# Kernel optimization log

Hardware: AMD Instinct MI355X
Metric: run time of the kernel (lower is better)

Reference implementation:

```python
import jax, jax.numpy as jnp
import numpy as np

N_RES = 768
C = 128  # act_dim == num_intermediate_channel
EPS = 1e-5


def _layer_norm(x, w, b):
    mu = jnp.mean(x, axis=-1, keepdims=True)
    var = jnp.mean(jnp.square(x - mu), axis=-1, keepdims=True)
    return (x - mu) * jax.lax.rsqrt(var + EPS) * w + b


def _linear(x, w, b):
    # torch Linear: w is [out, in]
    return jnp.einsum('ijc,dc->ijd', x, w) + b


def setup_inputs() -> dict:
    key = jax.random.key(0)
    ks = jax.random.split(key, 16)
    s = 1.0 / np.sqrt(C)
    d = {
        'act': jax.random.normal(ks[0], (N_RES, N_RES, C), jnp.float32),
        'mask': jnp.ones((N_RES, N_RES), jnp.float32),
        'ln_in_w': jnp.ones((C,), jnp.float32),
        'ln_in_b': jnp.zeros((C,), jnp.float32),
        'lp_w': jax.random.normal(ks[1], (C, C), jnp.float32) * s,
        'lp_b': jnp.zeros((C,), jnp.float32),
        'rp_w': jax.random.normal(ks[2], (C, C), jnp.float32) * s,
        'rp_b': jnp.zeros((C,), jnp.float32),
        'lg_w': jax.random.normal(ks[3], (C, C), jnp.float32) * s,
        'lg_b': jnp.ones((C,), jnp.float32),
        'rg_w': jax.random.normal(ks[4], (C, C), jnp.float32) * s,
        'rg_b': jnp.ones((C,), jnp.float32),
        'cln_w': jnp.ones((C,), jnp.float32),
        'cln_b': jnp.zeros((C,), jnp.float32),
        'op_w': jax.random.normal(ks[5], (C, C), jnp.float32) * s,
        'op_b': jnp.zeros((C,), jnp.float32),
        'gl_w': jax.random.normal(ks[6], (C, C), jnp.float32) * s,
        'gl_b': jnp.ones((C,), jnp.float32),
    }
    return d


def reference(act, mask, ln_in_w, ln_in_b, lp_w, lp_b, rp_w, rp_b,
              lg_w, lg_b, rg_w, rg_b, cln_w, cln_b, op_w, op_b, gl_w, gl_b):
    m = mask[..., None]                                   # [N, N, 1]
    act_ln = _layer_norm(act, ln_in_w, ln_in_b)           # [N, N, C]
    left = m * _linear(act_ln, lp_w, lp_b) * jax.nn.sigmoid(_linear(act_ln, lg_w, lg_b))
    right = m * _linear(act_ln, rp_w, rp_b) * jax.nn.sigmoid(_linear(act_ln, rg_w, rg_b))
    # outgoing-edges triangle multiplication
    out = jnp.einsum('ikc,jkc->ijc', left, right)          # [N, N, C]
    out = _layer_norm(out, cln_w, cln_b)
    out = _linear(out, op_w, op_b)
    gate = jax.nn.sigmoid(_linear(act_ln, gl_w, gl_b))
    return out * gate
```

## Files before the change

kernel.cpp:

```cpp
#include <hip/hip_runtime.h>
#include <hip/hip_bf16.h>
#include <math.h>


#define NRES 768
#define CD 128
#define NN (768 * 768)
#define PS2 (NN + 128)
#define PS4 (NN + 64)

typedef unsigned short u16;
typedef unsigned int u32;
typedef __attribute__((ext_vector_type(8))) short bf16x8;
typedef __attribute__((ext_vector_type(4))) float f32x4;

__device__ __forceinline__ float b2f(u16 u) {
  union { u32 i; float f; } v; v.i = ((u32)u) << 16; return v.f;
}
__device__ __forceinline__ u16 f2bf(float f) {
  __hip_bfloat16 h = __float2bfloat16(f);
  return *reinterpret_cast<u16*>(&h);
}
__device__ __forceinline__ float sigm(float x) {
  return __builtin_amdgcn_rcpf(1.0f + __builtin_amdgcn_exp2f(x * -1.44269504f));
}

__device__ __forceinline__ void async16(u16* lds, const u16* g) {
  __builtin_amdgcn_global_load_lds((const __attribute__((address_space(1))) void*)g,
                                   (__attribute__((address_space(3))) void*)lds, 16, 0, 0);
}

__device__ __forceinline__ void lds_fence() {
  asm volatile("s_waitcnt lgkmcnt(0)" ::: "memory");
  __builtin_amdgcn_sched_barrier(0);
}

__global__ void k_convw(const float* __restrict__ a, const float* __restrict__ b,
                        const float* __restrict__ c, const float* __restrict__ d,
                        const float* __restrict__ e, const float* __restrict__ f,
                        u16* __restrict__ wb) {
  int i = blockIdx.x * 256 + threadIdx.x;
  int m = i >> 14, r = i & 16383;
  const float* s = (m == 0) ? a : (m == 1) ? b : (m == 2) ? c : (m == 3) ? d : (m == 4) ? e : f;
  wb[i] = f2bf(s[r]);
}

__global__ __launch_bounds__(256, 3) void k_proj(
    const float* __restrict__ act, const float* __restrict__ mask,
    const float* __restrict__ lnw, const float* __restrict__ lnb,
    const u16* __restrict__ wb,
    const float* __restrict__ lpb, const float* __restrict__ lgb,
    const float* __restrict__ rpb, const float* __restrict__ rgb,
    const float* __restrict__ glb,
    u16* __restrict__ left_t, u16* __restrict__ right_t, u16* __restrict__ gate) {
  __shared__ u16 sx[128][128];
  __shared__ u16 stb[128 * 74];
  __shared__ float fmask[128];
  const int t = threadIdx.x;
  const int pos0 = blockIdx.x * 128;
  const int l = t & 63, w = t >> 6;
  const int lr = l & 15, g4 = l >> 4;

  {
    const int r = t >> 1, q = t & 1;
    const float* arow = act + (size_t)(pos0 + r) * CD + q * 64;
    float4 xv[16];
    float s = 0.f, ss = 0.f;
#pragma unroll
    for (int j = 0; j < 16; ++j) {
      xv[j] = *(const float4*)(arow + j * 4);
      s += xv[j].x + xv[j].y + xv[j].z + xv[j].w;
      ss += xv[j].x * xv[j].x + xv[j].y * xv[j].y + xv[j].z * xv[j].z + xv[j].w * xv[j].w;
    }
    s += __shfl_xor(s, 1); ss += __shfl_xor(ss, 1);
    float mu = s * (1.0f / CD);
    float rs = rsqrtf(ss * (1.0f / CD) - mu * mu + 1e-5f);
    const int key = (r & 7) << 3;
#pragma unroll
    for (int j = 0; j < 16; j += 2) {
      u16 o[8] __attribute__((aligned(16)));
      const float* xx = (const float*)&xv[j];
      int c0 = q * 64 + j * 4;
#pragma unroll
      for (int e2 = 0; e2 < 8; ++e2)
        o[e2] = f2bf((xx[e2] - mu) * rs * lnw[c0 + e2] + lnb[c0 + e2]);
      *(bf16x8*)&sx[r][c0 ^ key] = *(const bf16x8*)o;
    }
    if (t < 128) fmask[t] = mask[pos0 + t];
  }
  __syncthreads();

  auto pair_pass = [&](const u16* __restrict__ WP, const u16* __restrict__ WG,
                       const float* __restrict__ bP, const float* __restrict__ bG,
                       u16* __restrict__ dst) {
    bf16x8 bp[2][4], bg[2][4];
    float biasP[2], biasG[2];
    int dd[2];
#pragma unroll
    for (int c2 = 0; c2 < 2; ++c2) {
      dd[c2] = w * 32 + c2 * 16 + lr;
#pragma unroll
      for (int kk = 0; kk < 4; ++kk) {
        bp[c2][kk] = *(const bf16x8*)&WP[dd[c2] * CD + kk * 32 + g4 * 8];
        bg[c2][kk] = *(const bf16x8*)&WG[dd[c2] * CD + kk * 32 + g4 * 8];
      }
      biasP[c2] = bP[dd[c2]];
      biasG[c2] = bG[dd[c2]];
    }
#pragma unroll
    for (int mc = 0; mc < 2; ++mc) {
      lds_fence();
#pragma unroll
      for (int m = 0; m < 4; ++m) {
        const int row = mc * 64 + m * 16 + lr;
        const int key = (row & 7) << 3;
        bf16x8 af[4];
#pragma unroll
        for (int kk = 0; kk < 4; ++kk)
          af[kk] = *(const bf16x8*)&sx[row][(kk * 32 + g4 * 8) ^ key];
        const int rowc = m * 16 + g4 * 4;
        float fm[4];
#pragma unroll
        for (int r = 0; r < 4; ++r) fm[r] = fmask[mc * 64 + rowc + r];
#pragma unroll
        for (int c2 = 0; c2 < 2; ++c2) {
          f32x4 aP = {0.f, 0.f, 0.f, 0.f}, aG = {0.f, 0.f, 0.f, 0.f};
#pragma unroll
          for (int kk = 0; kk < 4; ++kk) {
            aP = __builtin_amdgcn_mfma_f32_16x16x32_bf16(af[kk], bp[c2][kk], aP, 0, 0, 0);
            aG = __builtin_amdgcn_mfma_f32_16x16x32_bf16(af[kk], bg[c2][kk], aG, 0, 0, 0);
          }
          u16 o[4] __attribute__((aligned(8)));
#pragma unroll
          for (int r = 0; r < 4; ++r)
            o[r] = f2bf((aP[r] + biasP[c2]) * sigm(aG[r] + biasG[c2]) * fm[r]);
          *(uint2*)&stb[dd[c2] * 74 + rowc] = *(const uint2*)o;
        }
      }
      lds_fence();
#pragma unroll
      for (int it = 0; it < 4; ++it) {
        const int d = w * 32 + it * 8 + (l >> 3), off = (l & 7) * 8;
        *(bf16x8*)&dst[(size_t)d * PS2 + pos0 + mc * 64 + off] = *(const bf16x8*)&stb[d * 74 + off];
      }
    }
  };

  pair_pass(wb, wb + 16384, lpb, lgb, left_t);
  pair_pass(wb + 2 * 16384, wb + 3 * 16384, rpb, rgb, right_t);

  __syncthreads();

  {
    const u16* WG = wb + 4 * 16384;
    bf16x8 bg[2][4];
    float biasG[2];
    int dd[2];
#pragma unroll
    for (int c2 = 0; c2 < 2; ++c2) {
      dd[c2] = w * 32 + c2 * 16 + lr;
#pragma unroll
      for (int kk = 0; kk < 4; ++kk)
        bg[c2][kk] = *(const bf16x8*)&WG[dd[c2] * CD + kk * 32 + g4 * 8];
      biasG[c2] = glb[dd[c2]];
    }
#pragma unroll
    for (int mc = 0; mc < 2; ++mc) {
#pragma unroll
      for (int m = 0; m < 4; ++m) {
        const int row = mc * 64 + m * 16 + lr;
        const int key = (row & 7) << 3;
        bf16x8 af[4];
#pragma unroll
        for (int kk = 0; kk < 4; ++kk)
          af[kk] = *(const bf16x8*)&sx[row][(kk * 32 + g4 * 8) ^ key];
        const int rowc = m * 16 + g4 * 4;
#pragma unroll
        for (int c2 = 0; c2 < 2; ++c2) {
          f32x4 aG = {0.f, 0.f, 0.f, 0.f};
#pragma unroll
          for (int kk = 0; kk < 4; ++kk)
            aG = __builtin_amdgcn_mfma_f32_16x16x32_bf16(af[kk], bg[c2][kk], aG, 0, 0, 0);
#pragma unroll
          for (int r = 0; r < 4; ++r)
            stb[(rowc + r) * 136 + dd[c2]] = f2bf(sigm(aG[r] + biasG[c2]));
        }
      }
      __syncthreads();
      {
        const int row = t >> 2, dc = (t & 3) * 32;
#pragma unroll
        for (int jj = 0; jj < 4; ++jj)
          *(bf16x8*)&gate[(size_t)(pos0 + mc * 64 + row) * CD + dc + jj * 8] =
              *(const bf16x8*)&stb[row * 136 + dc + jj * 8];
      }
      __syncthreads();
    }
  }
}

__global__ __launch_bounds__(256, 4) void k_tri(
    const u16* __restrict__ left_t, const u16* __restrict__ right_t,
    float* __restrict__ o1, float* __restrict__ o2, float* __restrict__ o3,
    int cbase) {
  __shared__ u16 sA[2][128 * 32];
  __shared__ u16 sB[2][128 * 32];
  const int t = threadIdx.x, l = t & 63, w = t >> 6;
  const int bid = blockIdx.x;
  const int xcd = bid & 7, idx = bid >> 3;
  const int c = cbase + xcd * 8 + idx / 36;
  const int tile = idx - (idx / 36) * 36;
  const int ti = tile / 6, tj = tile - (tile / 6) * 6;
  const u16* A = left_t + (size_t)c * PS2 + (size_t)ti * 128 * NRES;
  const u16* B = right_t + (size_t)c * PS2 + (size_t)tj * 128 * NRES;
  const int lr = l & 15, cj = l >> 4;
  const int wr = (w >> 1) * 64, wc = (w & 1) * 64;
  const int wbase = t & ~63;
  f32x4 acc[4][4];
#pragma unroll
  for (int m = 0; m < 4; ++m)
#pragma unroll
    for (int n = 0; n < 4; ++n) acc[m][n] = (f32x4){0.f, 0.f, 0.f, 0.f};

  auto stage = [&](int p, int k0) {
#pragma unroll
    for (int it = 0; it < 2; ++it) {
      int li = it * 256 + t;
      int row = li >> 2, ch = li & 3;
      int cs = ch ^ ((row >> 1) & 3);
      async16(&sA[p][(it * 256 + wbase) * 8], A + (size_t)row * NRES + k0 + cs * 8);
      async16(&sB[p][(it * 256 + wbase) * 8], B + (size_t)row * NRES + k0 + cs * 8);
    }
  };

  stage(0, 0);
  __syncthreads();
  for (int ks = 0; ks < 24; ++ks) {
    const int p = ks & 1;
    if (ks < 23) stage(p ^ 1, (ks + 1) * 32);
    bf16x8 av[4], bv[4];
#pragma unroll
    for (int m = 0; m < 4; ++m) {
      const int row = wr + m * 16 + lr;
      av[m] = *(const bf16x8*)&sA[p][row * 32 + ((cj ^ ((row >> 1) & 3)) * 8)];
    }
#pragma unroll
    for (int n = 0; n < 4; ++n) {
      const int row = wc + n * 16 + lr;
      bv[n] = *(const bf16x8*)&sB[p][row * 32 + ((cj ^ ((row >> 1) & 3)) * 8)];
    }
#pragma unroll
    for (int m = 0; m < 4; ++m)
#pragma unroll
      for (int n = 0; n < 4; ++n)
        acc[m][n] = __builtin_amdgcn_mfma_f32_16x16x32_bf16(av[m], bv[n], acc[m][n], 0, 0, 0);
    __syncthreads();
  }

  float* O = (c < 64) ? (o1 + (size_t)c * PS4)
           : (c < 96) ? (o2 + (size_t)(c - 64) * PS4)
                      : (o3 + (size_t)(c - 96) * PS4);
  const int r0l = (l >> 4) << 2;
#pragma unroll
  for (int m = 0; m < 4; ++m) {
#pragma unroll
    for (int n = 0; n < 4; ++n) {
      int row = ti * 128 + wr + m * 16 + r0l;
      int col = tj * 128 + wc + n * 16 + lr;
#pragma unroll
      for (int r = 0; r < 4; ++r)
        O[(size_t)(row + r) * NRES + col] = acc[m][n][r];
    }
  }
}

__global__ __launch_bounds__(256, 2) void k_post(
    const float* __restrict__ o1, const float* __restrict__ o2, const float* __restrict__ o3,
    const u16* __restrict__ gate,
    const float* __restrict__ clnw, const float* __restrict__ clnb,
    const u16* __restrict__ wop, const float* __restrict__ opb,
    float* __restrict__ out) {
  __shared__ u16 sx[256][128];
  __shared__ float ps[4][256];
  __shared__ float pss[4][256];
  __shared__ float mu_s[256], rs_s[256];
  const int t = threadIdx.x;
  const int pos0 = blockIdx.x * 256;
  const int l = t & 63, w = t >> 6;

  {
    const float* wbase = (w < 2) ? (o1 + (size_t)(w * 32) * PS4)
                       : (w == 2) ? o2 : o3;
    float s[4] = {0.f, 0.f, 0.f, 0.f}, ss[4] = {0.f, 0.f, 0.f, 0.f};
#pragma unroll
    for (int pp = 0; pp < 32; ++pp) {
      const float4 v = *(const float4*)&wbase[(size_t)pp * PS4 + pos0 + l * 4];
      s[0] += v.x; ss[0] += v.x * v.x;
      s[1] += v.y; ss[1] += v.y * v.y;
      s[2] += v.z; ss[2] += v.z * v.z;
      s[3] += v.w; ss[3] += v.w * v.w;
    }
#pragma unroll
    for (int e = 0; e < 4; ++e) {
      ps[w][l * 4 + e] = s[e];
      pss[w][l * 4 + e] = ss[e];
    }
  }
  __syncthreads();
  {
    const float s4 = ps[0][t] + ps[1][t] + ps[2][t] + ps[3][t];
    const float ss4 = pss[0][t] + pss[1][t] + pss[2][t] + pss[3][t];
    const float mu = s4 * (1.0f / CD);
    mu_s[t] = mu;
    rs_s[t] = rsqrtf(ss4 * (1.0f / CD) - mu * mu + 1e-5f);
  }
  __syncthreads();

  {
    const int q = t & 15, g = t >> 4;
    const int ch0 = q * 8;
    const float* base = (ch0 < 64) ? (o1 + (size_t)ch0 * PS4)
                      : (ch0 < 96) ? (o2 + (size_t)(ch0 - 64) * PS4)
                                   : (o3 + (size_t)(ch0 - 96) * PS4);
    float4 wv[2], bv[2];
#pragma unroll
    for (int j = 0; j < 2; ++j) {
      wv[j] = *(const float4*)&clnw[ch0 + j * 4];
      bv[j] = *(const float4*)&clnb[ch0 + j * 4];
    }
#pragma unroll
    for (int mc = 0; mc < 4; ++mc) {
      const int p0 = mc * 64 + g * 4;
      float4 x[8];
#pragma unroll
      for (int cc = 0; cc < 8; ++cc)
        x[cc] = *(const float4*)&base[(size_t)cc * PS4 + pos0 + p0];
#pragma unroll
      for (int e = 0; e < 4; ++e) {
        const int p = p0 + e;
        const float mu = mu_s[p], rs = rs_s[p];
        const int key = (p & 7) << 3;
        u16 o8[8] __attribute__((aligned(16)));
#pragma unroll
        for (int i = 0; i < 8; ++i) {
          const float xv = (e == 0) ? x[i].x : (e == 1) ? x[i].y : (e == 2) ? x[i].z : x[i].w;
          const float wvv = ((const float*)&wv[i >> 2])[i & 3];
          const float bvv = ((const float*)&bv[i >> 2])[i & 3];
          o8[i] = f2bf((xv - mu) * rs * wvv + bvv);
        }
        *(bf16x8*)&sx[p][ch0 ^ key] = *(const bf16x8*)o8;
      }
    }
  }
  __syncthreads();

  const int lr = l & 15, lk8 = (l >> 4) * 8;
  bf16x8 af[4][4];
#pragma unroll
  for (int m = 0; m < 4; ++m) {
    const int pr = w * 64 + m * 16 + lr;
    const int key = (pr & 7) << 3;
#pragma unroll
    for (int kk = 0; kk < 4; ++kk)
      af[m][kk] = *(const bf16x8*)&sx[pr][(kk * 32 + lk8) ^ key];
  }
  const int r0l = (l >> 4) << 2;
#pragma unroll
  for (int ct = 0; ct < 8; ++ct) {
    const int d = ct * 16 + lr;
    bf16x8 bv[4];
#pragma unroll
    for (int kk = 0; kk < 4; ++kk)
      bv[kk] = *(const bf16x8*)&wop[d * CD + kk * 32 + lk8];
    const float bo = opb[d];
#pragma unroll
    for (int m = 0; m < 4; ++m) {
      f32x4 acc = {0.f, 0.f, 0.f, 0.f};
#pragma unroll
      for (int kk = 0; kk < 4; ++kk)
        acc = __builtin_amdgcn_mfma_f32_16x16x32_bf16(af[m][kk], bv[kk], acc, 0, 0, 0);
      const int prow = w * 64 + m * 16 + r0l;
#pragma unroll
      for (int r = 0; r < 4; ++r) {
        size_t pp = (size_t)(pos0 + prow + r) * CD + d;
        out[pp] = (acc[r] + bo) * b2f(gate[pp]);
      }
    }
  }
}

extern "C" void kernel_launch(void* const* d_in, const int* in_sizes, int n_in,
                              void* d_out, int out_size, void* d_ws, size_t ws_size,
                              hipStream_t stream) {
  (void)in_sizes; (void)n_in; (void)out_size; (void)ws_size;
  const float* act  = (const float*)d_in[0];
  const float* mask = (const float*)d_in[1];
  const float* lnw  = (const float*)d_in[2];
  const float* lnb  = (const float*)d_in[3];
  const float* lpw  = (const float*)d_in[4];
  const float* lpb  = (const float*)d_in[5];
  const float* rpw  = (const float*)d_in[6];
  const float* rpb  = (const float*)d_in[7];
  const float* lgw  = (const float*)d_in[8];
  const float* lgb  = (const float*)d_in[9];
  const float* rgw  = (const float*)d_in[10];
  const float* rgb  = (const float*)d_in[11];
  const float* clnw = (const float*)d_in[12];
  const float* clnb = (const float*)d_in[13];
  const float* opw  = (const float*)d_in[14];
  const float* opb  = (const float*)d_in[15];
  const float* glw  = (const float*)d_in[16];
  const float* glb  = (const float*)d_in[17];

  char* wsb = (char*)d_ws;
  u16* wb = (u16*)wsb;
  const size_t RS = (size_t)128 * PS2 * 2;
  size_t off = (size_t)1 << 20;
  u16* left_t  = (u16*)(wsb + off); off += RS;
  u16* right_t = (u16*)(wsb + off); off += RS;
  u16* gate    = (u16*)(wsb + off); off += RS;
  float* o1    = (float*)(wsb + off); off += RS;
  float* o2    = (float*)left_t;
  float* o3    = (float*)right_t;

  k_convw<<<384, 256, 0, stream>>>(lpw, lgw, rpw, rgw, glw, opw, wb);
  k_proj<<<NN / 128, 256, 0, stream>>>(act, mask, lnw, lnb, wb,
                                       lpb, lgb, rpb, rgb, glb,
                                       left_t, right_t, gate);
  k_tri<<<2304, 256, 0, stream>>>(left_t, right_t, o1, o2, o3, 0);
  k_tri<<<2304, 256, 0, stream>>>(left_t, right_t, o1, o2, o3, 64);
  k_post<<<NN / 256, 256, 0, stream>>>(o1, o2, o3, gate, clnw, clnb,
                                       wb + 5 * 16384, opb, (float*)d_out);
}
```

Measured before the change: 684.3 us.

## Store left/right projections in 64-channel by 64-position blocked layout

The left and right projections were stored channel-major with one row per channel. They are now written as 4096-element blocks of 64 channels by 64 positions, with the two channel halves placed in separate regions. The proj kernel writes whole contiguous 8KB blocks, and the tri kernel reads each 64-position chunk through new block index arithmetic. The o2 and o3 aliases now point at the second half of each region. This is meant to make the proj stores contiguous, at the cost of tri reads touching 128-byte segments spread 8KB apart.

```diff
diff --git a/kernel.cpp b/kernel.cpp
--- a/kernel.cpp
+++ b/kernel.cpp
@@ -6,8 +6,8 @@
 #define NRES 768
 #define CD 128
 #define NN (768 * 768)
-#define PS2 (NN + 128)
 #define PS4 (NN + 64)
+#define HALFE ((size_t)9216 * 4096)
 
 typedef unsigned short u16;
 typedef unsigned int u32;
@@ -52,7 +52,7 @@
     const float* __restrict__ lpb, const float* __restrict__ lgb,
     const float* __restrict__ rpb, const float* __restrict__ rgb,
     const float* __restrict__ glb,
-    u16* __restrict__ left_t, u16* __restrict__ right_t, u16* __restrict__ gate) {
+    u16* __restrict__ left_s, u16* __restrict__ right_s, u16* __restrict__ gate) {
   __shared__ u16 sx[128][128];
   __shared__ u16 stb[128 * 74];
   __shared__ float fmask[128];
@@ -138,16 +138,19 @@
         }
       }
       lds_fence();
-#pragma unroll
-      for (int it = 0; it < 4; ++it) {
-        const int d = w * 32 + it * 8 + (l >> 3), off = (l & 7) * 8;
-        *(bf16x8*)&dst[(size_t)d * PS2 + pos0 + mc * 64 + off] = *(const bf16x8*)&stb[d * 74 + off];
+      {
+        u16* gdst = dst + ((w < 2) ? HALFE : (size_t)0) + (size_t)((pos0 >> 6) + mc) * 4096;
+#pragma unroll
+        for (int it = 0; it < 4; ++it) {
+          const int cc = w * 32 + it * 8 + (l >> 3), off = (l & 7) * 8;
+          *(bf16x8*)&gdst[(size_t)(cc & 63) * 64 + off] = *(const bf16x8*)&stb[cc * 74 + off];
+        }
       }
     }
   };
 
-  pair_pass(wb, wb + 16384, lpb, lgb, left_t);
-  pair_pass(wb + 2 * 16384, wb + 3 * 16384, rpb, rgb, right_t);
+  pair_pass(wb, wb + 16384, lpb, lgb, left_s);
+  pair_pass(wb + 2 * 16384, wb + 3 * 16384, rpb, rgb, right_s);
 
   __syncthreads();
 
@@ -200,7 +203,7 @@
 }
 
 __global__ __launch_bounds__(256, 4) void k_tri(
-    const u16* __restrict__ left_t, const u16* __restrict__ right_t,
+    const u16* __restrict__ left_s, const u16* __restrict__ right_s,
     float* __restrict__ o1, float* __restrict__ o2, float* __restrict__ o3,
     int cbase) {
   __shared__ u16 sA[2][128 * 32];
@@ -211,8 +214,9 @@
   const int c = cbase + xcd * 8 + idx / 36;
   const int tile = idx - (idx / 36) * 36;
   const int ti = tile / 6, tj = tile - (tile / 6) * 6;
-  const u16* A = left_t + (size_t)c * PS2 + (size_t)ti * 128 * NRES;
-  const u16* B = right_t + (size_t)c * PS2 + (size_t)tj * 128 * NRES;
+  const size_t hoff = (c < 64) ? HALFE : (size_t)0;
+  const u16* Abase = left_s + hoff + (size_t)(c & 63) * 64;
+  const u16* Bbase = right_s + hoff + (size_t)(c & 63) * 64;
   const int lr = l & 15, cj = l >> 4;
   const int wr = (w >> 1) * 64, wc = (w & 1) * 64;
   const int wbase = t & ~63;
@@ -223,13 +227,16 @@
     for (int n = 0; n < 4; ++n) acc[m][n] = (f32x4){0.f, 0.f, 0.f, 0.f};
 
   auto stage = [&](int p, int k0) {
+    const int gk = k0 >> 6, rk = k0 & 63;
 #pragma unroll
     for (int it = 0; it < 2; ++it) {
       int li = it * 256 + t;
       int row = li >> 2, ch = li & 3;
       int cs = ch ^ ((row >> 1) & 3);
-      async16(&sA[p][(it * 256 + wbase) * 8], A + (size_t)row * NRES + k0 + cs * 8);
-      async16(&sB[p][(it * 256 + wbase) * 8], B + (size_t)row * NRES + k0 + cs * 8);
+      async16(&sA[p][(it * 256 + wbase) * 8],
+              Abase + (size_t)((ti * 128 + row) * 12 + gk) * 4096 + rk + cs * 8);
+      async16(&sB[p][(it * 256 + wbase) * 8],
+              Bbase + (size_t)((tj * 128 + row) * 12 + gk) * 4096 + rk + cs * 8);
     }
   };
 
@@ -414,21 +421,21 @@
 
   char* wsb = (char*)d_ws;
   u16* wb = (u16*)wsb;
-  const size_t RS = (size_t)128 * PS2 * 2;
+  const size_t RS_LR = HALFE * 2 * 2 + 65536;
   size_t off = (size_t)1 << 20;
-  u16* left_t  = (u16*)(wsb + off); off += RS;
-  u16* right_t = (u16*)(wsb + off); off += RS;
-  u16* gate    = (u16*)(wsb + off); off += RS;
-  float* o1    = (float*)(wsb + off); off += RS;
-  float* o2    = (float*)left_t;
-  float* o3    = (float*)right_t;
+  u16* left_s  = (u16*)(wsb + off); off += RS_LR;
+  u16* right_s = (u16*)(wsb + off); off += RS_LR;
+  u16* gate    = (u16*)(wsb + off); off += (size_t)NN * CD * 2;
+  float* o1    = (float*)(wsb + off); off += (size_t)64 * PS4 * 4 + 65536;
+  float* o2    = (float*)(left_s + HALFE);
+  float* o3    = (float*)(right_s + HALFE);
 
   k_convw<<<384, 256, 0, stream>>>(lpw, lgw, rpw, rgw, glw, opw, wb);
   k_proj<<<NN / 128, 256, 0, stream>>>(act, mask, lnw, lnb, wb,
                                        lpb, lgb, rpb, rgb, glb,
-                                       left_t, right_t, gate);
-  k_tri<<<2304, 256, 0, stream>>>(left_t, right_t, o1, o2, o3, 0);
-  k_tri<<<2304, 256, 0, stream>>>(left_t, right_t, o1, o2, o3, 64);
+                                       left_s, right_s, gate);
+  k_tri<<<2304, 256, 0, stream>>>(left_s, right_s, o1, o2, o3, 0);
+  k_tri<<<2304, 256, 0, stream>>>(left_s, right_s, o1, o2, o3, 64);
   k_post<<<NN / 256, 256, 0, stream>>>(o1, o2, o3, gate, clnw, clnb,
                                        wb + 5 * 16384, opb, (float*)d_out);
 }
```

Result: slower. 734.8 us (+7.4%).

## Move gating linear from projection kernel into post kernel using stored LN activations

Applied to the files above, without the earlier changes.

The projection kernel no longer computes the sigmoid gate GEMM. Instead it writes the bf16 layer-normed input (act_ln) to the workspace, and the post kernel reloads it to compute the gate linear and sigmoid alongside the output projection. This shortens k_proj and removes its extra syncs and LDS staging. The cost is more MFMA work, registers and global fragment loads in k_post, which could lower its occupancy. Global traffic is about the same, since one bf16 tensor is written and read either way.

```diff
diff --git a/kernel.cpp b/kernel.cpp
--- a/kernel.cpp
+++ b/kernel.cpp
@@ -51,8 +51,7 @@
     const u16* __restrict__ wb,
     const float* __restrict__ lpb, const float* __restrict__ lgb,
     const float* __restrict__ rpb, const float* __restrict__ rgb,
-    const float* __restrict__ glb,
-    u16* __restrict__ left_t, u16* __restrict__ right_t, u16* __restrict__ gate) {
+    u16* __restrict__ left_t, u16* __restrict__ right_t, u16* __restrict__ actln) {
   __shared__ u16 sx[128][128];
   __shared__ u16 stb[128 * 74];
   __shared__ float fmask[128];
@@ -90,6 +89,18 @@
   }
   __syncthreads();
 
+#pragma unroll
+  for (int it = 0; it < 2; ++it) {
+    const int row = it * 64 + (t >> 2);
+    const int key = (row & 7) << 3;
+    const int dc = (t & 3) * 32;
+#pragma unroll
+    for (int jj = 0; jj < 4; ++jj) {
+      const int c0 = dc + jj * 8;
+      *(bf16x8*)&actln[(size_t)(pos0 + row) * CD + c0] = *(const bf16x8*)&sx[row][c0 ^ key];
+    }
+  }
+
   auto pair_pass = [&](const u16* __restrict__ WP, const u16* __restrict__ WG,
                        const float* __restrict__ bP, const float* __restrict__ bG,
                        u16* __restrict__ dst) {
@@ -148,55 +159,6 @@
 
   pair_pass(wb, wb + 16384, lpb, lgb, left_t);
   pair_pass(wb + 2 * 16384, wb + 3 * 16384, rpb, rgb, right_t);
-
-  __syncthreads();
-
-  {
-    const u16* WG = wb + 4 * 16384;
-    bf16x8 bg[2][4];
-    float biasG[2];
-    int dd[2];
-#pragma unroll
-    for (int c2 = 0; c2 < 2; ++c2) {
-      dd[c2] = w * 32 + c2 * 16 + lr;
-#pragma unroll
-      for (int kk = 0; kk < 4; ++kk)
-        bg[c2][kk] = *(const bf16x8*)&WG[dd[c2] * CD + kk * 32 + g4 * 8];
-      biasG[c2] = glb[dd[c2]];
-    }
-#pragma unroll
-    for (int mc = 0; mc < 2; ++mc) {
-#pragma unroll
-      for (int m = 0; m < 4; ++m) {
-        const int row = mc * 64 + m * 16 + lr;
-        const int key = (row & 7) << 3;
-        bf16x8 af[4];
-#pragma unroll
-        for (int kk = 0; kk < 4; ++kk)
-          af[kk] = *(const bf16x8*)&sx[row][(kk * 32 + g4 * 8) ^ key];
-        const int rowc = m * 16 + g4 * 4;
-#pragma unroll
-        for (int c2 = 0; c2 < 2; ++c2) {
-          f32x4 aG = {0.f, 0.f, 0.f, 0.f};
-#pragma unroll
-          for (int kk = 0; kk < 4; ++kk)
-            aG = __builtin_amdgcn_mfma_f32_16x16x32_bf16(af[kk], bg[c2][kk], aG, 0, 0, 0);
-#pragma unroll
-          for (int r = 0; r < 4; ++r)
-            stb[(rowc + r) * 136 + dd[c2]] = f2bf(sigm(aG[r] + biasG[c2]));
-        }
-      }
-      __syncthreads();
-      {
-        const int row = t >> 2, dc = (t & 3) * 32;
-#pragma unroll
-        for (int jj = 0; jj < 4; ++jj)
-          *(bf16x8*)&gate[(size_t)(pos0 + mc * 64 + row) * CD + dc + jj * 8] =
-              *(const bf16x8*)&stb[row * 136 + dc + jj * 8];
-      }
-      __syncthreads();
-    }
-  }
 }
 
 __global__ __launch_bounds__(256, 4) void k_tri(
@@ -276,9 +238,10 @@
 
 __global__ __launch_bounds__(256, 2) void k_post(
     const float* __restrict__ o1, const float* __restrict__ o2, const float* __restrict__ o3,
-    const u16* __restrict__ gate,
+    const u16* __restrict__ actln,
     const float* __restrict__ clnw, const float* __restrict__ clnb,
-    const u16* __restrict__ wop, const float* __restrict__ opb,
+    const u16* __restrict__ wop, const u16* __restrict__ wgl,
+    const float* __restrict__ opb, const float* __restrict__ glb,
     float* __restrict__ out) {
   __shared__ u16 sx[256][128];
   __shared__ float ps[4][256];
@@ -355,35 +318,42 @@
   __syncthreads();
 
   const int lr = l & 15, lk8 = (l >> 4) * 8;
-  bf16x8 af[4][4];
+  bf16x8 af[4][4], af2[4][4];
 #pragma unroll
   for (int m = 0; m < 4; ++m) {
     const int pr = w * 64 + m * 16 + lr;
     const int key = (pr & 7) << 3;
 #pragma unroll
-    for (int kk = 0; kk < 4; ++kk)
+    for (int kk = 0; kk < 4; ++kk) {
       af[m][kk] = *(const bf16x8*)&sx[pr][(kk * 32 + lk8) ^ key];
+      af2[m][kk] = *(const bf16x8*)&actln[(size_t)(pos0 + pr) * CD + kk * 32 + lk8];
+    }
   }
   const int r0l = (l >> 4) << 2;
 #pragma unroll
   for (int ct = 0; ct < 8; ++ct) {
     const int d = ct * 16 + lr;
-    bf16x8 bv[4];
-#pragma unroll
-    for (int kk = 0; kk < 4; ++kk)
+    bf16x8 bv[4], bgl[4];
+#pragma unroll
+    for (int kk = 0; kk < 4; ++kk) {
       bv[kk] = *(const bf16x8*)&wop[d * CD + kk * 32 + lk8];
+      bgl[kk] = *(const bf16x8*)&wgl[d * CD + kk * 32 + lk8];
+    }
     const float bo = opb[d];
+    const float bgb = glb[d];
 #pragma unroll
     for (int m = 0; m < 4; ++m) {
-      f32x4 acc = {0.f, 0.f, 0.f, 0.f};
-#pragma unroll
-      for (int kk = 0; kk < 4; ++kk)
+      f32x4 acc = {0.f, 0.f, 0.f, 0.f}, gacc = {0.f, 0.f, 0.f, 0.f};
+#pragma unroll
+      for (int kk = 0; kk < 4; ++kk) {
         acc = __builtin_amdgcn_mfma_f32_16x16x32_bf16(af[m][kk], bv[kk], acc, 0, 0, 0);
+        gacc = __builtin_amdgcn_mfma_f32_16x16x32_bf16(af2[m][kk], bgl[kk], gacc, 0, 0, 0);
+      }
       const int prow = w * 64 + m * 16 + r0l;
 #pragma unroll
       for (int r = 0; r < 4; ++r) {
         size_t pp = (size_t)(pos0 + prow + r) * CD + d;
-        out[pp] = (acc[r] + bo) * b2f(gate[pp]);
+        out[pp] = (acc[r] + bo) * sigm(gacc[r] + bgb);
       }
     }
   }
@@ -418,17 +388,18 @@
   size_t off = (size_t)1 << 20;
   u16* left_t  = (u16*)(wsb + off); off += RS;
   u16* right_t = (u16*)(wsb + off); off += RS;
-  u16* gate    = (u16*)(wsb + off); off += RS;
+  u16* actln   = (u16*)(wsb + off); off += RS;
   float* o1    = (float*)(wsb + off); off += RS;
   float* o2    = (float*)left_t;
   float* o3    = (float*)right_t;
 
   k_convw<<<384, 256, 0, stream>>>(lpw, lgw, rpw, rgw, glw, opw, wb);
   k_proj<<<NN / 128, 256, 0, stream>>>(act, mask, lnw, lnb, wb,
-                                       lpb, lgb, rpb, rgb, glb,
-                                       left_t, right_t, gate);
+                                       lpb, lgb, rpb, rgb,
+                                       left_t, right_t, actln);
   k_tri<<<2304, 256, 0, stream>>>(left_t, right_t, o1, o2, o3, 0);
   k_tri<<<2304, 256, 0, stream>>>(left_t, right_t, o1, o2, o3, 64);
-  k_post<<<NN / 256, 256, 0, stream>>>(o1, o2, o3, gate, clnw, clnb,
-                                       wb + 5 * 16384, opb, (float*)d_out);
-}
+  k_post<<<NN / 256, 256, 0, stream>>>(o1, o2, o3, actln, clnw, clnb,
+                                       wb + 5 * 16384, wb + 4 * 16384,
+                                       opb, glb, (float*)d_out);
+}
```

New measurement: 700.8 us. +2.4%, slower.
